# Kernel optimization log

Hardware: AMD Instinct MI355X
Metric: run time of the kernel (lower is better)

The kernel has to match this reference:

```python
import jax, jax.numpy as jnp
import numpy as np

NEG_SLOPE = 0.2  # PyG GATConv default


def gat_conv(x, edge_index, W, a_src, a_dst, bias):
    """Single-head PyG-style GATConv (eval mode, add_self_loops=True)."""
    N = x.shape[0]
    h = x @ W  # [N, F_out]
    # add self loops
    loops = jnp.arange(N, dtype=edge_index.dtype)
    src = jnp.concatenate([edge_index[0], loops])  # [E+N]
    dst = jnp.concatenate([edge_index[1], loops])
    # per-edge attention logits: a_src . h_j + a_dst . h_i  (j=src, i=dst)
    alpha_s = h @ a_src  # [N]
    alpha_d = h @ a_dst  # [N]
    e = jax.nn.leaky_relu(alpha_s[src] + alpha_d[dst], NEG_SLOPE)  # [E+N]
    # segment softmax over incoming edges of each dst node
    m = jax.ops.segment_max(e, dst, num_segments=N)
    ex = jnp.exp(e - m[dst])
    denom = jax.ops.segment_sum(ex, dst, num_segments=N)
    alpha = ex / denom[dst]  # [E+N]
    # weighted scatter-aggregate of source features
    out = jax.ops.segment_sum(h[src] * alpha[:, None], dst, num_segments=N)
    return out + bias


def setup_inputs() -> dict:
    key = jax.random.key(0)
    ks = jax.random.split(key, 12)
    N, E = 100000, 3200000
    Fin, H, Fout = 128, 32, 32
    x = jax.random.normal(ks[0], (N, Fin), dtype=jnp.float32)
    edge_index = jax.random.randint(ks[1], (2, E), 0, N, dtype=jnp.int64)
    s = 1.0 / np.sqrt(Fin)
    W1 = jax.random.uniform(ks[2], (Fin, H), jnp.float32, -s, s)
    a1s = jax.random.uniform(ks[3], (H,), jnp.float32, -s, s)
    a1d = jax.random.uniform(ks[4], (H,), jnp.float32, -s, s)
    b1 = jnp.zeros((H,), jnp.float32)
    s2 = 1.0 / np.sqrt(H)
    W2 = jax.random.uniform(ks[5], (H, H), jnp.float32, -s2, s2)
    a2s = jax.random.uniform(ks[6], (H,), jnp.float32, -s2, s2)
    a2d = jax.random.uniform(ks[7], (H,), jnp.float32, -s2, s2)
    b2 = jnp.zeros((H,), jnp.float32)
    Wf = jax.random.uniform(ks[8], (H, Fout), jnp.float32, -s2, s2)
    bf = jax.random.uniform(ks[9], (Fout,), jnp.float32, -s2, s2)
    return {"x": x, "edge_index": edge_index, "W1": W1, "a1s": a1s, "a1d": a1d,
            "b1": b1, "W2": W2, "a2s": a2s, "a2d": a2d, "b2": b2,
            "Wf": Wf, "bf": bf}


def reference(x, edge_index, W1, a1s, a1d, b1, W2, a2s, a2d, b2, Wf, bf):
    h = jax.nn.relu(gat_conv(x, edge_index, W1, a1s, a1d, b1))
    h = jax.nn.relu(gat_conv(h, edge_index, W2, a2s, a2d, b2))
    return h @ Wf + bf
```

## Files before the change

### kernel.cpp

```cpp
#include <hip/hip_runtime.h>

#define NEG_SLOPE 0.2f
#define BK_LOG 9
#define BK_NODES (1 << BK_LOG)
#define TILE_EPT 24
#define TILE_E (256 * TILE_EPT)

typedef __attribute__((ext_vector_type(8))) short bf8_t;
typedef __attribute__((ext_vector_type(4))) float f32x4;

__device__ __forceinline__ float leaky(float v) { return v > 0.0f ? v : NEG_SLOPE * v; }

__device__ __forceinline__ unsigned short f2bf(float f) {
    unsigned u = __float_as_uint(f);
    u += 0x7fffu + ((u >> 16) & 1u);
    return (unsigned short)(u >> 16);
}
__device__ __forceinline__ float bf2f(unsigned short h) {
    return __uint_as_float(((unsigned)h) << 16);
}

__device__ __forceinline__ int scan256_excl(int v, int* tmp) {
    int t = threadIdx.x;
    tmp[t] = v;
    __syncthreads();
    for (int d = 1; d < 256; d <<= 1) {
        int x = (t >= d) ? tmp[t - d] : 0;
        __syncthreads();
        tmp[t] += x;
        __syncthreads();
    }
    int r = tmp[t] - v;
    __syncthreads();
    return r;
}


__global__ __launch_bounds__(256) void k_bzero(int* __restrict__ bcnt) {
    bcnt[threadIdx.x] = 0;
}

__global__ __launch_bounds__(256) void k_bcount(const int* __restrict__ edst,
                                                int* __restrict__ bcnt, int E) {
    __shared__ int th[256];
    int t = threadIdx.x;
    th[t] = 0;
    __syncthreads();
    int base = blockIdx.x * TILE_E;
#pragma unroll
    for (int k = 0; k < TILE_EPT; ++k) {
        int e = base + t + k * 256;
        if (e < E) atomicAdd(&th[edst[e] >> BK_LOG], 1);
    }
    __syncthreads();
    if (th[t]) atomicAdd(&bcnt[t], th[t]);
}

__global__ __launch_bounds__(256) void k_bscan(const int* __restrict__ bcnt,
                                               int* __restrict__ bbase,
                                               int* __restrict__ bcur,
                                               int* __restrict__ off, int N, int E) {
    __shared__ int tmp[256];
    int t = threadIdx.x;
    int ex = scan256_excl(bcnt[t], tmp);
    bbase[t] = ex;
    bcur[t]  = ex;
    if (t == 0) { bbase[256] = E; off[N] = E; }
}

__global__ __launch_bounds__(256) void k_bplace(const int* __restrict__ esrc,
                                                const int* __restrict__ edst,
                                                int* __restrict__ bcur,
                                                int2* __restrict__ pairs, int E) {
    __shared__ int2 sp[TILE_E];
    __shared__ int th[256], tx[256], rb[256], tmp[256];
    int t = threadIdx.x;
    th[t] = 0;
    __syncthreads();
    int base = blockIdx.x * TILE_E;
    int tot  = min(TILE_E, E - base);
#pragma unroll
    for (int k = 0; k < TILE_EPT; ++k) {
        int e = base + t + k * 256;
        if (e < E) atomicAdd(&th[edst[e] >> BK_LOG], 1);
    }
    __syncthreads();
    int cnt = th[t];
    tx[t] = scan256_excl(cnt, tmp);
    rb[t] = atomicAdd(&bcur[t], cnt);
    th[t] = 0;
    __syncthreads();
#pragma unroll
    for (int k = 0; k < TILE_EPT; ++k) {
        int e = base + t + k * 256;
        if (e < E) {
            int s = esrc[e], d = edst[e];
            int b = d >> BK_LOG;
            int r = atomicAdd(&th[b], 1);
            sp[tx[b] + r] = make_int2(s, d);
        }
    }
    __syncthreads();
    for (int i = t; i < tot; i += 256) {
        int2 p = sp[i];
        int  b = p.y >> BK_LOG;
        pairs[rb[b] + (i - tx[b])] = p;
    }
}

__global__ __launch_bounds__(256) void k_csr(const int* __restrict__ bbase,
                                             const int2* __restrict__ pairs,
                                             int* __restrict__ off,
                                             int* __restrict__ csr, int N) {
    __shared__ int lh[BK_NODES], lx[BK_NODES];
    int b = blockIdx.x, t = threadIdx.x;
    int lo = bbase[b], hi = bbase[b + 1];
    int node0 = b << BK_LOG;
    lh[t] = 0; lh[t + 256] = 0;
    __syncthreads();
    for (int j = lo + t; j < hi; j += 256)
        atomicAdd(&lh[pairs[j].y - node0], 1);
    __syncthreads();
    lx[t] = lh[t]; lx[t + 256] = lh[t + 256];
    __syncthreads();
    for (int d = 1; d < BK_NODES; d <<= 1) {
        int i1 = t + 256;
        int x0 = (t  >= d) ? lx[t  - d] : 0;
        int x1 = (i1 >= d) ? lx[i1 - d] : 0;
        __syncthreads();
        lx[t] += x0; lx[i1] += x1;
        __syncthreads();
    }
    lx[t] -= lh[t]; lx[t + 256] -= lh[t + 256];
    if (node0 + t       < N) off[node0 + t]       = lo + lx[t];
    if (node0 + t + 256 < N) off[node0 + t + 256] = lo + lx[t + 256];
    lh[t] = 0; lh[t + 256] = 0;
    __syncthreads();
    for (int j = lo + t; j < hi; j += 256) {
        int2 p  = pairs[j];
        int  li = p.y - node0;
        int  r  = atomicAdd(&lh[li], 1);
        csr[lo + lx[li] + r] = p.x;
    }
}

__global__ __launch_bounds__(256) void k_wsplit(const float* __restrict__ W,
                                                unsigned short* __restrict__ wh,
                                                unsigned short* __restrict__ wl,
                                                int K) {
    int idx = blockIdx.x * 256 + threadIdx.x;
    int KT = K >> 5;
    if (idx >= KT * 128) return;
    int lane = idx & 63;
    int nt = (idx >> 6) & 1;
    int kt = idx >> 7;
    int q = lane >> 4, c = lane & 15;
#pragma unroll
    for (int j = 0; j < 8; ++j) {
        int k = kt * 32 + q * 8 + j;
        int n = nt * 16 + c;
        float w = W[k * 32 + n];
        unsigned short hi = f2bf(w);
        wh[idx * 8 + j] = hi;
        wl[idx * 8 + j] = f2bf(w - bf2f(hi));
    }
}

template <int FIN, bool ATT>
__global__ __launch_bounds__(256) void gemm_mfma(
    const float* __restrict__ x,
    const unsigned short* __restrict__ wh, const unsigned short* __restrict__ wl,
    const float* __restrict__ a_s, const float* __restrict__ a_d,
    const float* __restrict__ bias,
    float* __restrict__ h, float* __restrict__ alpha_s,
    float* __restrict__ alpha_d, int N)
{
    constexpr int KT = FIN / 32;
    int lane = threadIdx.x & 63;
    int mt   = blockIdx.x * 4 + (threadIdx.x >> 6);
    int m0   = mt * 16;
    if (m0 >= N) return;
    int q = lane >> 4, c = lane & 15;

    bf8_t Bh[KT][2], Bl[KT][2];
#pragma unroll
    for (int kt = 0; kt < KT; ++kt)
#pragma unroll
        for (int nt = 0; nt < 2; ++nt) {
            Bh[kt][nt] = *(const bf8_t*)(wh + ((size_t)(kt * 2 + nt) * 64 + lane) * 8);
            Bl[kt][nt] = *(const bf8_t*)(wl + ((size_t)(kt * 2 + nt) * 64 + lane) * 8);
        }

    int rowa = m0 + c;
    if (rowa >= N) rowa = N - 1;
    const float* xr = x + (size_t)rowa * FIN;
    bf8_t Ah[KT], Al[KT];
#pragma unroll
    for (int kt = 0; kt < KT; ++kt) {
        f32x4 v0 = *(const f32x4*)(xr + kt * 32 + q * 8);
        f32x4 v1 = *(const f32x4*)(xr + kt * 32 + q * 8 + 4);
#pragma unroll
        for (int j = 0; j < 8; ++j) {
            float f = (j < 4) ? v0[j] : v1[j - 4];
            unsigned short hi = f2bf(f);
            Ah[kt][j] = (short)hi;
            Al[kt][j] = (short)f2bf(f - bf2f(hi));
        }
    }

    f32x4 acc0 = {0.f, 0.f, 0.f, 0.f}, acc1 = {0.f, 0.f, 0.f, 0.f};
#pragma unroll
    for (int kt = 0; kt < KT; ++kt) {
        acc0 = __builtin_amdgcn_mfma_f32_16x16x32_bf16(Ah[kt], Bh[kt][0], acc0, 0, 0, 0);
        acc1 = __builtin_amdgcn_mfma_f32_16x16x32_bf16(Ah[kt], Bh[kt][1], acc1, 0, 0, 0);
        acc0 = __builtin_amdgcn_mfma_f32_16x16x32_bf16(Al[kt], Bh[kt][0], acc0, 0, 0, 0);
        acc1 = __builtin_amdgcn_mfma_f32_16x16x32_bf16(Al[kt], Bh[kt][1], acc1, 0, 0, 0);
        acc0 = __builtin_amdgcn_mfma_f32_16x16x32_bf16(Ah[kt], Bl[kt][0], acc0, 0, 0, 0);
        acc1 = __builtin_amdgcn_mfma_f32_16x16x32_bf16(Ah[kt], Bl[kt][1], acc1, 0, 0, 0);
    }

#pragma unroll
    for (int reg = 0; reg < 4; ++reg) {
        int r = m0 + q * 4 + reg;
        if (r < N) {
            float v0s = acc0[reg], v1s = acc1[reg];
            if (!ATT) { v0s += bias[c]; v1s += bias[c + 16]; }
            h[(size_t)r * 32 + c]      = v0s;
            h[(size_t)r * 32 + 16 + c] = v1s;
        }
    }
    if (ATT) {
        float as0 = a_s[c], as1 = a_s[c + 16];
        float ad0 = a_d[c], ad1 = a_d[c + 16];
#pragma unroll
        for (int reg = 0; reg < 4; ++reg) {
            float ps = acc0[reg] * as0 + acc1[reg] * as1;
            float pd = acc0[reg] * ad0 + acc1[reg] * ad1;
#pragma unroll
            for (int msk = 8; msk >= 1; msk >>= 1) {
                ps += __shfl_xor(ps, msk);
                pd += __shfl_xor(pd, msk);
            }
            int r = m0 + q * 4 + reg;
            if (c == 0 && r < N) {
                alpha_s[r] = ps;
                alpha_d[r] = pd;
            }
        }
    }
}

__global__ __launch_bounds__(256) void fused_agg(
    const int* __restrict__ csr, const int* __restrict__ off,
    const float* __restrict__ alpha_s, const float* __restrict__ alpha_d,
    const float* __restrict__ h, const float* __restrict__ bias,
    float* __restrict__ out, int N)
{
    int t = blockIdx.x * 256 + threadIdx.x;
    int i = t >> 3, q = t & 7;
    if (i >= N) return;
    int s0 = off[i], s1 = off[i + 1];
    float ad = alpha_d[i];

    const float* hq = h + q * 4;

    float w   = __expf(leaky(alpha_s[i] + ad));
    float den = w;
    f32x4 hv  = *(const f32x4*)(hq + (size_t)i * 32);
    f32x4 acc;
    acc[0] = w * hv[0]; acc[1] = w * hv[1]; acc[2] = w * hv[2]; acc[3] = w * hv[3];

    int j = s0;
    for (; j + 8 <= s1; j += 8) {
        int   c  = csr[j + q];
        float wv = __expf(leaky(alpha_s[c] + ad));
        int   co = c << 5;
#pragma unroll
        for (int e = 0; e < 8; ++e) {
            int   ce = __shfl(co, e, 8);
            float we = __shfl(wv, e, 8);
            f32x4 hg = *(const f32x4*)(hq + ce);
            den += we;
            acc[0] += we * hg[0]; acc[1] += we * hg[1];
            acc[2] += we * hg[2]; acc[3] += we * hg[3];
        }
    }
    int rem = s1 - j;
    if (rem > 0) {
        int c = 0; float wv = 0.0f;
        if (q < rem) {
            c  = csr[j + q];
            wv = __expf(leaky(alpha_s[c] + ad));
        }
        int co = c << 5;
        for (int e = 0; e < rem; ++e) {
            int   ce = __shfl(co, e, 8);
            float we = __shfl(wv, e, 8);
            f32x4 hg = *(const f32x4*)(hq + ce);
            den += we;
            acc[0] += we * hg[0]; acc[1] += we * hg[1];
            acc[2] += we * hg[2]; acc[3] += we * hg[3];
        }
    }

    float inv = 1.0f / den;
    f32x4 b4  = *(const f32x4*)(bias + q * 4);
    f32x4 r;
    r[0] = fmaxf(acc[0] * inv + b4[0], 0.0f);
    r[1] = fmaxf(acc[1] * inv + b4[1], 0.0f);
    r[2] = fmaxf(acc[2] * inv + b4[2], 0.0f);
    r[3] = fmaxf(acc[3] * inv + b4[3], 0.0f);
    *(f32x4*)(out + (size_t)i * 32 + q * 4) = r;
}

extern "C" void kernel_launch(void* const* d_in, const int* in_sizes, int n_in,
                              void* d_out, int out_size, void* d_ws, size_t ws_size,
                              hipStream_t stream)
{
    const float* x   = (const float*)d_in[0];
    const int*   ei  = (const int*)d_in[1];
    const float* W1  = (const float*)d_in[2];
    const float* a1s = (const float*)d_in[3];
    const float* a1d = (const float*)d_in[4];
    const float* b1  = (const float*)d_in[5];
    const float* W2  = (const float*)d_in[6];
    const float* a2s = (const float*)d_in[7];
    const float* a2d = (const float*)d_in[8];
    const float* b2  = (const float*)d_in[9];
    const float* Wf  = (const float*)d_in[10];
    const float* bf  = (const float*)d_in[11];

    const int N = in_sizes[0] / 128;
    const int E = in_sizes[1] / 2;
    const int* esrc = ei;
    const int* edst = ei + E;
    const int B1 = (N + BK_NODES - 1) >> BK_LOG;

    float* ws = (float*)d_ws;
    float* h1      = ws;
    float* h2      = h1 + (size_t)N * 32;
    float* alpha_s = h2 + (size_t)N * 32;
    float* alpha_d = alpha_s + N;
    int*   off     = (int*)(alpha_d + N);
    int*   csr     = off + (N + 1);
    int*   bcnt    = csr + E;
    int*   bbase   = bcnt + 256;
    int*   bcur    = bbase + 257;
    unsigned short* wfb =
        (unsigned short*)(((uintptr_t)(bcur + 256) + 15) & ~(uintptr_t)15);
    unsigned short* wh1 = wfb;
    unsigned short* wl1 = wh1 + 4096;
    unsigned short* wh2 = wl1 + 4096;
    unsigned short* wl2 = wh2 + 1024;
    unsigned short* whf = wl2 + 1024;
    unsigned short* wlf = whf + 1024;
    int2* pairs = ((size_t)2 * E <= (size_t)64 * N)
                      ? (int2*)h1
                      : (int2*)(wlf + 1024);

    const int nb_agg  = (N * 8 + 255) / 256;
    const int nb_tile = (E + TILE_E - 1) / TILE_E;
    const int nb_gemm = ((N + 15) / 16 + 3) / 4;

    k_wsplit<<<2, 256, 0, stream>>>(W1, wh1, wl1, 128);
    k_wsplit<<<1, 256, 0, stream>>>(W2, wh2, wl2, 32);
    k_wsplit<<<1, 256, 0, stream>>>(Wf, whf, wlf, 32);

    k_bzero  <<<1, 256, 0, stream>>>(bcnt);
    k_bcount <<<nb_tile, 256, 0, stream>>>(edst, bcnt, E);
    k_bscan  <<<1, 256, 0, stream>>>(bcnt, bbase, bcur, off, N, E);
    k_bplace <<<nb_tile, 256, 0, stream>>>(esrc, edst, bcur, pairs, E);
    k_csr    <<<B1, 256, 0, stream>>>(bbase, pairs, off, csr, N);

    gemm_mfma<128, true><<<nb_gemm, 256, 0, stream>>>(
        x, wh1, wl1, a1s, a1d, nullptr, h1, alpha_s, alpha_d, N);
    fused_agg<<<nb_agg, 256, 0, stream>>>(csr, off, alpha_s, alpha_d, h1, b1, h2, N);

    gemm_mfma<32, true><<<nb_gemm, 256, 0, stream>>>(
        h2, wh2, wl2, a2s, a2d, nullptr, h1, alpha_s, alpha_d, N);
    fused_agg<<<nb_agg, 256, 0, stream>>>(csr, off, alpha_s, alpha_d, h1, b2, h2, N);

    gemm_mfma<32, false><<<nb_gemm, 256, 0, stream>>>(
        h2, whf, wlf, nullptr, nullptr, bf, (float*)d_out, nullptr, nullptr, N);
}
```

Measured before the change: 365.9 us.

## Pack bucketed edge pairs into 32-bit words and unroll aggregation gather by four

Edge pairs written by the bucket-place pass are packed into a single 32-bit word (source index shifted plus local destination offset) instead of an int2, halving the intermediate traffic between k_bplace and k_csr. k_csr now runs 512 threads per bucket, one per local node, which simplifies the scan. The aggregation kernel adds a 32-edge unrolled loop that issues four independent feature gathers per step to raise memory-level parallelism. The packing assumes source indices fit in 23 bits, and the unroll increases register pressure.

```diff
diff --git a/kernel.cpp b/kernel.cpp
--- a/kernel.cpp
+++ b/kernel.cpp
@@ -71,7 +71,7 @@
 __global__ __launch_bounds__(256) void k_bplace(const int* __restrict__ esrc,
                                                 const int* __restrict__ edst,
                                                 int* __restrict__ bcur,
-                                                int2* __restrict__ pairs, int E) {
+                                                unsigned* __restrict__ pairs, int E) {
     __shared__ int2 sp[TILE_E];
     __shared__ int th[256], tx[256], rb[256], tmp[256];
     int t = threadIdx.x;
@@ -104,43 +104,41 @@
     for (int i = t; i < tot; i += 256) {
         int2 p = sp[i];
         int  b = p.y >> BK_LOG;
-        pairs[rb[b] + (i - tx[b])] = p;
-    }
-}
-
-__global__ __launch_bounds__(256) void k_csr(const int* __restrict__ bbase,
-                                             const int2* __restrict__ pairs,
+        pairs[rb[b] + (i - tx[b])] =
+            ((unsigned)p.x << BK_LOG) | (unsigned)(p.y & (BK_NODES - 1));
+    }
+}
+
+__global__ __launch_bounds__(512) void k_csr(const int* __restrict__ bbase,
+                                             const unsigned* __restrict__ pairs,
                                              int* __restrict__ off,
                                              int* __restrict__ csr, int N) {
     __shared__ int lh[BK_NODES], lx[BK_NODES];
     int b = blockIdx.x, t = threadIdx.x;
     int lo = bbase[b], hi = bbase[b + 1];
     int node0 = b << BK_LOG;
-    lh[t] = 0; lh[t + 256] = 0;
-    __syncthreads();
-    for (int j = lo + t; j < hi; j += 256)
-        atomicAdd(&lh[pairs[j].y - node0], 1);
-    __syncthreads();
-    lx[t] = lh[t]; lx[t + 256] = lh[t + 256];
+    lh[t] = 0;
+    __syncthreads();
+    for (int j = lo + t; j < hi; j += 512)
+        atomicAdd(&lh[pairs[j] & (BK_NODES - 1)], 1);
+    __syncthreads();
+    lx[t] = lh[t];
     __syncthreads();
     for (int d = 1; d < BK_NODES; d <<= 1) {
-        int i1 = t + 256;
-        int x0 = (t  >= d) ? lx[t  - d] : 0;
-        int x1 = (i1 >= d) ? lx[i1 - d] : 0;
+        int x0 = (t >= d) ? lx[t - d] : 0;
         __syncthreads();
-        lx[t] += x0; lx[i1] += x1;
+        lx[t] += x0;
         __syncthreads();
     }
-    lx[t] -= lh[t]; lx[t + 256] -= lh[t + 256];
-    if (node0 + t       < N) off[node0 + t]       = lo + lx[t];
-    if (node0 + t + 256 < N) off[node0 + t + 256] = lo + lx[t + 256];
-    lh[t] = 0; lh[t + 256] = 0;
-    __syncthreads();
-    for (int j = lo + t; j < hi; j += 256) {
-        int2 p  = pairs[j];
-        int  li = p.y - node0;
-        int  r  = atomicAdd(&lh[li], 1);
-        csr[lo + lx[li] + r] = p.x;
+    lx[t] -= lh[t];
+    if (node0 + t < N) off[node0 + t] = lo + lx[t];
+    lh[t] = 0;
+    __syncthreads();
+    for (int j = lo + t; j < hi; j += 512) {
+        unsigned p  = pairs[j];
+        int      li = p & (BK_NODES - 1);
+        int      r  = atomicAdd(&lh[li], 1);
+        csr[lo + lx[li] + r] = (int)(p >> BK_LOG);
     }
 }
 
@@ -271,6 +269,38 @@
     acc[0] = w * hv[0]; acc[1] = w * hv[1]; acc[2] = w * hv[2]; acc[3] = w * hv[3];
 
     int j = s0;
+    for (; j + 32 <= s1; j += 32) {
+        int c0 = csr[j + q];
+        int c1 = csr[j + 8 + q];
+        int c2 = csr[j + 16 + q];
+        int c3 = csr[j + 24 + q];
+        float a0 = alpha_s[c0], a1 = alpha_s[c1], a2 = alpha_s[c2], a3 = alpha_s[c3];
+        float w0 = __expf(leaky(a0 + ad));
+        float w1 = __expf(leaky(a1 + ad));
+        float w2 = __expf(leaky(a2 + ad));
+        float w3 = __expf(leaky(a3 + ad));
+        int o0 = c0 << 5, o1 = c1 << 5, o2 = c2 << 5, o3 = c3 << 5;
+#pragma unroll
+        for (int e = 0; e < 8; ++e) {
+            int   e0 = __shfl(o0, e, 8); float f0 = __shfl(w0, e, 8);
+            int   e1 = __shfl(o1, e, 8); float f1 = __shfl(w1, e, 8);
+            int   e2 = __shfl(o2, e, 8); float f2 = __shfl(w2, e, 8);
+            int   e3 = __shfl(o3, e, 8); float f3 = __shfl(w3, e, 8);
+            f32x4 g0 = *(const f32x4*)(hq + e0);
+            f32x4 g1 = *(const f32x4*)(hq + e1);
+            f32x4 g2 = *(const f32x4*)(hq + e2);
+            f32x4 g3 = *(const f32x4*)(hq + e3);
+            den += (f0 + f1) + (f2 + f3);
+            acc[0] += f0 * g0[0]; acc[1] += f0 * g0[1];
+            acc[2] += f0 * g0[2]; acc[3] += f0 * g0[3];
+            acc[0] += f1 * g1[0]; acc[1] += f1 * g1[1];
+            acc[2] += f1 * g1[2]; acc[3] += f1 * g1[3];
+            acc[0] += f2 * g2[0]; acc[1] += f2 * g2[1];
+            acc[2] += f2 * g2[2]; acc[3] += f2 * g2[3];
+            acc[0] += f3 * g3[0]; acc[1] += f3 * g3[1];
+            acc[2] += f3 * g3[2]; acc[3] += f3 * g3[3];
+        }
+    }
     for (; j + 8 <= s1; j += 8) {
         int   c  = csr[j + q];
         float wv = __expf(leaky(alpha_s[c] + ad));
@@ -354,9 +384,9 @@
     unsigned short* wl2 = wh2 + 1024;
     unsigned short* whf = wl2 + 1024;
     unsigned short* wlf = whf + 1024;
-    int2* pairs = ((size_t)2 * E <= (size_t)64 * N)
-                      ? (int2*)h1
-                      : (int2*)(wlf + 1024);
+    unsigned* pairs = ((size_t)E <= (size_t)64 * N)
+                          ? (unsigned*)h1
+                          : (unsigned*)(wlf + 1024);
 
     const int nb_agg  = (N * 8 + 255) / 256;
     const int nb_tile = (E + TILE_E - 1) / TILE_E;
@@ -370,7 +400,7 @@
     k_bcount <<<nb_tile, 256, 0, stream>>>(edst, bcnt, E);
     k_bscan  <<<1, 256, 0, stream>>>(bcnt, bbase, bcur, off, N, E);
     k_bplace <<<nb_tile, 256, 0, stream>>>(esrc, edst, bcur, pairs, E);
-    k_csr    <<<B1, 256, 0, stream>>>(bbase, pairs, off, csr, N);
+    k_csr    <<<B1, 512, 0, stream>>>(bbase, pairs, off, csr, N);
 
     gemm_mfma<128, true><<<nb_gemm, 256, 0, stream>>>(
         x, wh1, wl1, a1s, a1d, nullptr, h1, alpha_s, alpha_d, N);
```

Result: faster. 353.3 us (-3.4%).
